# Optimization experiments

Hardware: AMD Instinct MI355X
Metric: run time of the kernel (lower is better)

## Reference

```python
import jax, jax.numpy as jnp
import numpy as np

D_MODEL = 512
EPS = 1e-5


def setup_inputs() -> dict:
    key = jax.random.key(0)
    k1, k2, k3 = jax.random.split(key, 3)
    B, N, D = 8, 2048, D_MODEL
    output = jax.random.normal(k1, (B, N, D), dtype=jnp.float32)
    # multiplicative 0/1 float mask over the [B, N, N] score matrix
    slf_attn_mask = jax.random.randint(k2, (B, N, N), 0, 2).astype(jnp.float32)
    # nn.Linear(d_model, d_model): weight [out, in], xavier-uniform; bias zeros-ish
    limit = float(np.sqrt(6.0 / (D + D)))
    W = jax.random.uniform(k3, (D, D), dtype=jnp.float32, minval=-limit, maxval=limit)
    b = jnp.zeros((D,), dtype=jnp.float32)
    return {"output": output, "slf_attn_mask": slf_attn_mask, "W": W, "b": b}


def reference(output, slf_attn_mask, W, b):
    temperature = jnp.asarray(D_MODEL, output.dtype) ** 0.5
    # scores: [B, N, N] = (q / temp) @ k^T, then multiplicative mask
    attn = jnp.einsum("bnd,bmd->bnm", output / temperature, output) * slf_attn_mask
    # F.normalize(p=2, dim=-1, eps=1e-5): x / max(||x||_2, eps)
    norm = jnp.sqrt(jnp.sum(attn * attn, axis=-1, keepdims=True))
    attn = attn / jnp.maximum(norm, EPS)
    # values: elu(Linear(output)), Linear uses W @ x + b with W [out, in]
    v = jax.nn.elu(jnp.einsum("bnd,ed->bne", output, W) + b)
    return jnp.einsum("bnm,bme->bne", attn, v)
```

## Files before the change

kernel.cpp:

```cpp
#include <hip/hip_runtime.h>
#include <hip/hip_bf16.h>

#define NSEQ 2048
#define DM 512
#define BATCH 8
#define GTOT (BATCH * NSEQ)
#define INV_T 0.044194173824159216f
#define EPSN 1e-5f

typedef __bf16 bf16_t;
typedef bf16_t bf16x8 __attribute__((ext_vector_type(8)));
typedef float f32x16 __attribute__((ext_vector_type(16)));
typedef unsigned short u16;
typedef unsigned int u32;
typedef unsigned char u8;
typedef unsigned long long u64;

__device__ __forceinline__ u16 f2bf(float f) {
    u32 u = __builtin_bit_cast(u32, f);
    u32 r = (u + 0x7FFFu + ((u >> 16) & 1u)) >> 16;
    return (u16)r;
}

__device__ __forceinline__ void async16(const u16* g, u16* l) {
    __builtin_amdgcn_global_load_lds(
        (const __attribute__((address_space(1))) u32*)g,
        (__attribute__((address_space(3))) u32*)l, 16, 0, 0);
}

__device__ __forceinline__ bf16x8 fragld64(const u16* t, int row, int kc) {
    return *(const bf16x8*)(t + row * 64 + ((kc ^ ((row >> 1) & 7)) << 3));
}

#define MFMA32(a, b, c) __builtin_amdgcn_mfma_f32_32x32x16_bf16(a, b, c, 0, 0, 0)
#define ROWOFF(reg, lh) (((reg) & 3) + 8 * ((reg) >> 2) + 4 * (lh))

#define STAGE64(Ag, ldA, Bg, ldB, k0)                                            \
    do {                                                                         \
        _Pragma("unroll") for (int j = 0; j < 4; ++j) {                          \
            const int cg = (lane & 7) ^ ((j * 4 + (lane >> 4)) & 7);             \
            const int dst = (wave * 4 + j) * 512 + lane * 8;                     \
            async16((Ag) + (long)(rS + j * 8) * (ldA) + (k0) + cg * 8, Ab + dst);\
            async16((Bg) + (long)(rS + j * 8) * (ldB) + (k0) + cg * 8, Bb + dst);\
        }                                                                        \
    } while (0)

__global__ __launch_bounds__(256) void k_convert(
    const float* __restrict__ X, const float* __restrict__ W,
    u16* __restrict__ Kbf, u16* __restrict__ Wbf, float* __restrict__ ssbuf) {
    const long NK = (long)GTOT * DM / 4;
    const long NW = (long)DM * DM / 4;
    const long NS = GTOT / 4;
    long i = (long)blockIdx.x * 256 + threadIdx.x;
    if (i < NK) {
        float4 f = ((const float4*)X)[i];
        ushort4 o;
        o.x = f2bf(f.x); o.y = f2bf(f.y); o.z = f2bf(f.z); o.w = f2bf(f.w);
        ((ushort4*)Kbf)[i] = o;
    } else if (i < NK + NW) {
        long j = i - NK;
        float4 f = ((const float4*)W)[j];
        ushort4 o;
        o.x = f2bf(f.x); o.y = f2bf(f.y); o.z = f2bf(f.z); o.w = f2bf(f.w);
        ((ushort4*)Wbf)[j] = o;
    } else if (i < NK + NW + NS) {
        ((float4*)ssbuf)[i - NK - NW] = (float4){0.f, 0.f, 0.f, 0.f};
    }
}

__global__ __launch_bounds__(256) void k_maskpack(
    const float* __restrict__ mask, u64* __restrict__ Mbits) {
    __shared__ u8 nib[256];
    const int tid = threadIdx.x;
    const long fbase = (long)blockIdx.x * 256 + tid;
    float4 f = ((const float4*)mask)[fbase];
    unsigned n = (f.x != 0.f ? 1u : 0u) | (f.y != 0.f ? 2u : 0u) |
                 (f.z != 0.f ? 4u : 0u) | (f.w != 0.f ? 8u : 0u);
    nib[tid] = (u8)n;
    __syncthreads();
    if (tid < 16) {
        u64 w = 0;
#pragma unroll
        for (int i = 0; i < 16; ++i) w |= (u64)nib[tid * 16 + i] << (i * 4);
        Mbits[(long)blockIdx.x * 16 + tid] = w;
    }
}

__global__ __launch_bounds__(256, 4) void k_sgemm(
    const u16* __restrict__ Kbf, const u32* __restrict__ Mw,
    u16* __restrict__ Sbuf, float* __restrict__ ssbuf) {
    __shared__ __attribute__((aligned(16))) u16 Ab[8192], Bb[8192];
    const int tid = threadIdx.x, wave = tid >> 6, lane = tid & 63;
    const int l31 = lane & 31, lh = lane >> 5;
    const int wy = wave >> 1, wx = wave & 1;
    const int b = blockIdx.z;
    const int M0 = blockIdx.y * 128, N0 = blockIdx.x * 128;
    const u16* Ag = Kbf + (long)(b * NSEQ + M0) * DM;
    const u16* Bg = Kbf + (long)(b * NSEQ + N0) * DM;
    const u32* Mb = Mw + (long)b * NSEQ * 64;

    const int rS = wave * 32 + (lane >> 3);

    f32x16 acc[2][2];
#pragma unroll
    for (int i = 0; i < 2; ++i)
#pragma unroll
        for (int j = 0; j < 2; ++j)
#pragma unroll
            for (int e = 0; e < 16; ++e) acc[i][j][e] = 0.f;

    for (int kt = 0; kt < 8; ++kt) {
        const int k0 = kt * 64;
        __syncthreads();
        STAGE64(Ag, DM, Bg, DM, k0);
        __syncthreads();
#pragma unroll
        for (int ks = 0; ks < 4; ++ks) {
            const int kc = ks * 2 + lh;
            bf16x8 a0 = fragld64(Ab, wy * 64 + l31, kc);
            bf16x8 a1 = fragld64(Ab, wy * 64 + 32 + l31, kc);
            bf16x8 b0 = fragld64(Bb, wx * 64 + l31, kc);
            bf16x8 b1 = fragld64(Bb, wx * 64 + 32 + l31, kc);
            acc[0][0] = MFMA32(a0, b0, acc[0][0]);
            acc[0][1] = MFMA32(a0, b1, acc[0][1]);
            acc[1][0] = MFMA32(a1, b0, acc[1][0]);
            acc[1][1] = MFMA32(a1, b1, acc[1][1]);
        }
    }
#pragma unroll
    for (int mi = 0; mi < 2; ++mi) {
#pragma unroll
        for (int reg = 0; reg < 16; ++reg) {
            int rl = M0 + wy * 64 + mi * 32 + ROWOFF(reg, lh);
            long rg = (long)b * NSEQ + rl;
            float v = 0.f;
#pragma unroll
            for (int ni = 0; ni < 2; ++ni) {
                int cg = N0 + wx * 64 + ni * 32 + l31;
                u32 w = Mb[(long)rl * 64 + (cg >> 5)];
                float s = ((w >> l31) & 1u) ? acc[mi][ni][reg] * INV_T : 0.f;
                v += s * s;
                Sbuf[rg * NSEQ + cg] = f2bf(s);
            }
            v += __shfl_xor(v, 1, 32);
            v += __shfl_xor(v, 2, 32);
            v += __shfl_xor(v, 4, 32);
            v += __shfl_xor(v, 8, 32);
            v += __shfl_xor(v, 16, 32);
            if (l31 == 0) atomicAdd(&ssbuf[rg], v);
        }
    }
}

__global__ __launch_bounds__(256, 4) void k_vgemm(
    const u16* __restrict__ Wbf, const u16* __restrict__ Kbf,
    const float* __restrict__ bias, u16* __restrict__ vT) {
    __shared__ __attribute__((aligned(16))) u16 Ab[8192], Bb[8192];
    const int tid = threadIdx.x, wave = tid >> 6, lane = tid & 63;
    const int l31 = lane & 31, lh = lane >> 5;
    const int wy = wave >> 1, wx = wave & 1;
    const int M0 = blockIdx.y * 128, N0 = blockIdx.x * 128;
    const u16* Ag = Wbf + (long)M0 * DM;
    const u16* Bg = Kbf + (long)N0 * DM;

    const int rS = wave * 32 + (lane >> 3);

    f32x16 acc[2][2];
#pragma unroll
    for (int i = 0; i < 2; ++i)
#pragma unroll
        for (int j = 0; j < 2; ++j)
#pragma unroll
            for (int e = 0; e < 16; ++e) acc[i][j][e] = 0.f;

    for (int kt = 0; kt < 8; ++kt) {
        const int k0 = kt * 64;
        __syncthreads();
        STAGE64(Ag, DM, Bg, DM, k0);
        __syncthreads();
#pragma unroll
        for (int ks = 0; ks < 4; ++ks) {
            const int kc = ks * 2 + lh;
            bf16x8 a0 = fragld64(Ab, wy * 64 + l31, kc);
            bf16x8 a1 = fragld64(Ab, wy * 64 + 32 + l31, kc);
            bf16x8 b0 = fragld64(Bb, wx * 64 + l31, kc);
            bf16x8 b1 = fragld64(Bb, wx * 64 + 32 + l31, kc);
            acc[0][0] = MFMA32(a0, b0, acc[0][0]);
            acc[0][1] = MFMA32(a0, b1, acc[0][1]);
            acc[1][0] = MFMA32(a1, b0, acc[1][0]);
            acc[1][1] = MFMA32(a1, b1, acc[1][1]);
        }
    }
#pragma unroll
    for (int mi = 0; mi < 2; ++mi) {
#pragma unroll
        for (int reg = 0; reg < 16; ++reg) {
            int e = M0 + wy * 64 + mi * 32 + ROWOFF(reg, lh);
            float bv = bias[e];
#pragma unroll
            for (int ni = 0; ni < 2; ++ni) {
                int g = N0 + wx * 64 + ni * 32 + l31;
                float x = acc[mi][ni][reg] + bv;
                float v = x > 0.f ? x : (__expf(x) - 1.f);
                vT[(long)e * GTOT + g] = f2bf(v);
            }
        }
    }
}

__global__ __launch_bounds__(256, 4) void k_pv(
    const u16* __restrict__ Sbuf, const u16* __restrict__ vT,
    const float* __restrict__ ssbuf, float* __restrict__ Out) {
    __shared__ __attribute__((aligned(16))) u16 Ab[8192], Bb[8192];
    __shared__ float sc[128];
    const int tid = threadIdx.x, wave = tid >> 6, lane = tid & 63;
    const int l31 = lane & 31, lh = lane >> 5;
    const int wy = wave >> 1, wx = wave & 1;
    const int b = blockIdx.z;
    const int M0 = blockIdx.y * 128, N0 = blockIdx.x * 128;
    const u16* Ag = Sbuf + (long)(b * NSEQ + M0) * NSEQ;
    const u16* Bg = vT + (long)N0 * GTOT + b * NSEQ;

    if (tid < 128) {
        float v = ssbuf[b * NSEQ + M0 + tid];
        sc[tid] = 1.f / fmaxf(sqrtf(v), EPSN);
    }

    const int rS = wave * 32 + (lane >> 3);

    f32x16 acc[2][2];
#pragma unroll
    for (int i = 0; i < 2; ++i)
#pragma unroll
        for (int j = 0; j < 2; ++j)
#pragma unroll
            for (int e = 0; e < 16; ++e) acc[i][j][e] = 0.f;

    for (int kt = 0; kt < 32; ++kt) {
        const int k0 = kt * 64;
        __syncthreads();
        STAGE64(Ag, NSEQ, Bg, GTOT, k0);
        __syncthreads();
#pragma unroll
        for (int ks = 0; ks < 4; ++ks) {
            const int kc = ks * 2 + lh;
            bf16x8 a0 = fragld64(Ab, wy * 64 + l31, kc);
            bf16x8 a1 = fragld64(Ab, wy * 64 + 32 + l31, kc);
            bf16x8 b0 = fragld64(Bb, wx * 64 + l31, kc);
            bf16x8 b1 = fragld64(Bb, wx * 64 + 32 + l31, kc);
            acc[0][0] = MFMA32(a0, b0, acc[0][0]);
            acc[0][1] = MFMA32(a0, b1, acc[0][1]);
            acc[1][0] = MFMA32(a1, b0, acc[1][0]);
            acc[1][1] = MFMA32(a1, b1, acc[1][1]);
        }
    }
#pragma unroll
    for (int mi = 0; mi < 2; ++mi) {
#pragma unroll
        for (int reg = 0; reg < 16; ++reg) {
            int rl = wy * 64 + mi * 32 + ROWOFF(reg, lh);
            float s = sc[rl];
            float* op = Out + ((long)b * NSEQ + M0 + rl) * DM;
#pragma unroll
            for (int ni = 0; ni < 2; ++ni) {
                int d = N0 + wx * 64 + ni * 32 + l31;
                op[d] = acc[mi][ni][reg] * s;
            }
        }
    }
}

extern "C" void kernel_launch(void* const* d_in, const int* in_sizes, int n_in,
                              void* d_out, int out_size, void* d_ws, size_t ws_size,
                              hipStream_t stream) {
    const float* X = (const float*)d_in[0];
    const float* mask = (const float*)d_in[1];
    const float* W = (const float*)d_in[2];
    const float* bias = (const float*)d_in[3];
    float* out = (float*)d_out;

    char* ws = (char*)d_ws;
    u16* Kbf = (u16*)ws;
    u16* Wbf = (u16*)(ws + 16777216);
    u16* vT = (u16*)(ws + 17301504);
    u16* Sbuf = (u16*)(ws + 34078720);
    float* ssbuf = (float*)(ws + 101187584);
    u64* Mbits = (u64*)(ws + 101253120);

    k_convert<<<8464, 256, 0, stream>>>(X, W, Kbf, Wbf, ssbuf);
    k_maskpack<<<32768, 256, 0, stream>>>(mask, Mbits);
    k_vgemm<<<dim3(128, 4), 256, 0, stream>>>(Wbf, Kbf, bias, vT);
    k_sgemm<<<dim3(16, 16, 8), 256, 0, stream>>>(Kbf, (const u32*)Mbits, Sbuf, ssbuf);
    k_pv<<<dim3(4, 16, 8), 256, 0, stream>>>(Sbuf, vT, ssbuf, out);
}
```

Baseline: 347.8 us.

## Fuse score GEMM, masking, row-norm and PV GEMM into one kernel

Replaces the separate score GEMM and PV GEMM kernels with a single fused kernel where each block holds 64 query rows in LDS, computes masked scores for 256-key chunks, stages them as bf16 in LDS, and immediately multiplies by V. Row sums of squares are accumulated in registers and reduced across waves at the end, removing the global score buffer round-trip and the atomics. The trade-off is a grid of only 256 large blocks with K and V fragments loaded directly from global memory without double buffering, which may expose latency.

Measured after the change: 396.1 us. 1.14x slower.

```diff
diff --git a/kernel.cpp b/kernel.cpp
--- a/kernel.cpp
+++ b/kernel.cpp
@@ -47,10 +47,9 @@
 
 __global__ __launch_bounds__(256) void k_convert(
     const float* __restrict__ X, const float* __restrict__ W,
-    u16* __restrict__ Kbf, u16* __restrict__ Wbf, float* __restrict__ ssbuf) {
+    u16* __restrict__ Kbf, u16* __restrict__ Wbf) {
     const long NK = (long)GTOT * DM / 4;
     const long NW = (long)DM * DM / 4;
-    const long NS = GTOT / 4;
     long i = (long)blockIdx.x * 256 + threadIdx.x;
     if (i < NK) {
         float4 f = ((const float4*)X)[i];
@@ -63,8 +62,6 @@
         ushort4 o;
         o.x = f2bf(f.x); o.y = f2bf(f.y); o.z = f2bf(f.z); o.w = f2bf(f.w);
         ((ushort4*)Wbf)[j] = o;
-    } else if (i < NK + NW + NS) {
-        ((float4*)ssbuf)[i - NK - NW] = (float4){0.f, 0.f, 0.f, 0.f};
     }
 }
 
@@ -86,18 +83,16 @@
     }
 }
 
-__global__ __launch_bounds__(256, 4) void k_sgemm(
-    const u16* __restrict__ Kbf, const u32* __restrict__ Mw,
-    u16* __restrict__ Sbuf, float* __restrict__ ssbuf) {
+__global__ __launch_bounds__(256, 4) void k_vgemm(
+    const u16* __restrict__ Wbf, const u16* __restrict__ Kbf,
+    const float* __restrict__ bias, u16* __restrict__ vT) {
     __shared__ __attribute__((aligned(16))) u16 Ab[8192], Bb[8192];
     const int tid = threadIdx.x, wave = tid >> 6, lane = tid & 63;
     const int l31 = lane & 31, lh = lane >> 5;
     const int wy = wave >> 1, wx = wave & 1;
-    const int b = blockIdx.z;
     const int M0 = blockIdx.y * 128, N0 = blockIdx.x * 128;
-    const u16* Ag = Kbf + (long)(b * NSEQ + M0) * DM;
-    const u16* Bg = Kbf + (long)(b * NSEQ + N0) * DM;
-    const u32* Mb = Mw + (long)b * NSEQ * 64;
+    const u16* Ag = Wbf + (long)M0 * DM;
+    const u16* Bg = Kbf + (long)N0 * DM;
 
     const int rS = wave * 32 + (lane >> 3);
 
@@ -131,70 +126,6 @@
     for (int mi = 0; mi < 2; ++mi) {
 #pragma unroll
         for (int reg = 0; reg < 16; ++reg) {
-            int rl = M0 + wy * 64 + mi * 32 + ROWOFF(reg, lh);
-            long rg = (long)b * NSEQ + rl;
-            float v = 0.f;
-#pragma unroll
-            for (int ni = 0; ni < 2; ++ni) {
-                int cg = N0 + wx * 64 + ni * 32 + l31;
-                u32 w = Mb[(long)rl * 64 + (cg >> 5)];
-                float s = ((w >> l31) & 1u) ? acc[mi][ni][reg] * INV_T : 0.f;
-                v += s * s;
-                Sbuf[rg * NSEQ + cg] = f2bf(s);
-            }
-            v += __shfl_xor(v, 1, 32);
-            v += __shfl_xor(v, 2, 32);
-            v += __shfl_xor(v, 4, 32);
-            v += __shfl_xor(v, 8, 32);
-            v += __shfl_xor(v, 16, 32);
-            if (l31 == 0) atomicAdd(&ssbuf[rg], v);
-        }
-    }
-}
-
-__global__ __launch_bounds__(256, 4) void k_vgemm(
-    const u16* __restrict__ Wbf, const u16* __restrict__ Kbf,
-    const float* __restrict__ bias, u16* __restrict__ vT) {
-    __shared__ __attribute__((aligned(16))) u16 Ab[8192], Bb[8192];
-    const int tid = threadIdx.x, wave = tid >> 6, lane = tid & 63;
-    const int l31 = lane & 31, lh = lane >> 5;
-    const int wy = wave >> 1, wx = wave & 1;
-    const int M0 = blockIdx.y * 128, N0 = blockIdx.x * 128;
-    const u16* Ag = Wbf + (long)M0 * DM;
-    const u16* Bg = Kbf + (long)N0 * DM;
-
-    const int rS = wave * 32 + (lane >> 3);
-
-    f32x16 acc[2][2];
-#pragma unroll
-    for (int i = 0; i < 2; ++i)
-#pragma unroll
-        for (int j = 0; j < 2; ++j)
-#pragma unroll
-            for (int e = 0; e < 16; ++e) acc[i][j][e] = 0.f;
-
-    for (int kt = 0; kt < 8; ++kt) {
-        const int k0 = kt * 64;
-        __syncthreads();
-        STAGE64(Ag, DM, Bg, DM, k0);
-        __syncthreads();
-#pragma unroll
-        for (int ks = 0; ks < 4; ++ks) {
-            const int kc = ks * 2 + lh;
-            bf16x8 a0 = fragld64(Ab, wy * 64 + l31, kc);
-            bf16x8 a1 = fragld64(Ab, wy * 64 + 32 + l31, kc);
-            bf16x8 b0 = fragld64(Bb, wx * 64 + l31, kc);
-            bf16x8 b1 = fragld64(Bb, wx * 64 + 32 + l31, kc);
-            acc[0][0] = MFMA32(a0, b0, acc[0][0]);
-            acc[0][1] = MFMA32(a0, b1, acc[0][1]);
-            acc[1][0] = MFMA32(a1, b0, acc[1][0]);
-            acc[1][1] = MFMA32(a1, b1, acc[1][1]);
-        }
-    }
-#pragma unroll
-    for (int mi = 0; mi < 2; ++mi) {
-#pragma unroll
-        for (int reg = 0; reg < 16; ++reg) {
             int e = M0 + wy * 64 + mi * 32 + ROWOFF(reg, lh);
             float bv = bias[e];
 #pragma unroll
@@ -208,64 +139,132 @@
     }
 }
 
-__global__ __launch_bounds__(256, 4) void k_pv(
-    const u16* __restrict__ Sbuf, const u16* __restrict__ vT,
-    const float* __restrict__ ssbuf, float* __restrict__ Out) {
-    __shared__ __attribute__((aligned(16))) u16 Ab[8192], Bb[8192];
-    __shared__ float sc[128];
-    const int tid = threadIdx.x, wave = tid >> 6, lane = tid & 63;
-    const int l31 = lane & 31, lh = lane >> 5;
-    const int wy = wave >> 1, wx = wave & 1;
-    const int b = blockIdx.z;
-    const int M0 = blockIdx.y * 128, N0 = blockIdx.x * 128;
-    const u16* Ag = Sbuf + (long)(b * NSEQ + M0) * NSEQ;
-    const u16* Bg = vT + (long)N0 * GTOT + b * NSEQ;
-
-    if (tid < 128) {
-        float v = ssbuf[b * NSEQ + M0 + tid];
-        sc[tid] = 1.f / fmaxf(sqrtf(v), EPSN);
-    }
-
-    const int rS = wave * 32 + (lane >> 3);
-
-    f32x16 acc[2][2];
+__global__ __launch_bounds__(512, 2) void k_fused(
+    const u16* __restrict__ Kbf, const u16* __restrict__ vT,
+    const u32* __restrict__ Mw, float* __restrict__ Out) {
+    __shared__ __attribute__((aligned(16))) u16 Qb[64 * 512];
+    __shared__ __attribute__((aligned(16))) u16 Sb[64 * 256];
+    __shared__ float ssred[8][64];
+    __shared__ float ssinv[64];
+
+    const int tid = threadIdx.x;
+    const int w = tid >> 6, lane = tid & 63, l31 = lane & 31, lh = lane >> 5;
+    const int b = blockIdx.x & 7, q = blockIdx.x >> 3;
+    const int M0 = q * 64;
+    const long rowbase = (long)b * NSEQ + M0;
+
+    {
+        const u16* src = Kbf + rowbase * DM;
+#pragma unroll
+        for (int it = 0; it < 8; ++it) {
+            int idx = it * 512 + tid;
+            int row = idx >> 6, cd = idx & 63;
+            int cg = cd ^ (row & 31);
+            async16(src + (long)row * DM + cg * 8, Qb + idx * 8);
+        }
+    }
+
+    f32x16 oc[2][2];
 #pragma unroll
     for (int i = 0; i < 2; ++i)
 #pragma unroll
         for (int j = 0; j < 2; ++j)
 #pragma unroll
-            for (int e = 0; e < 16; ++e) acc[i][j][e] = 0.f;
-
-    for (int kt = 0; kt < 32; ++kt) {
-        const int k0 = kt * 64;
-        __syncthreads();
-        STAGE64(Ag, NSEQ, Bg, GTOT, k0);
-        __syncthreads();
-#pragma unroll
-        for (int ks = 0; ks < 4; ++ks) {
-            const int kc = ks * 2 + lh;
-            bf16x8 a0 = fragld64(Ab, wy * 64 + l31, kc);
-            bf16x8 a1 = fragld64(Ab, wy * 64 + 32 + l31, kc);
-            bf16x8 b0 = fragld64(Bb, wx * 64 + l31, kc);
-            bf16x8 b1 = fragld64(Bb, wx * 64 + 32 + l31, kc);
-            acc[0][0] = MFMA32(a0, b0, acc[0][0]);
-            acc[0][1] = MFMA32(a0, b1, acc[0][1]);
-            acc[1][0] = MFMA32(a1, b0, acc[1][0]);
-            acc[1][1] = MFMA32(a1, b1, acc[1][1]);
-        }
-    }
-#pragma unroll
-    for (int mi = 0; mi < 2; ++mi) {
+            for (int e = 0; e < 16; ++e) oc[i][j][e] = 0.f;
+
+    float ss[32];
+#pragma unroll
+    for (int i = 0; i < 32; ++i) ss[i] = 0.f;
+
+    const u16* kp = Kbf + ((long)b * NSEQ + 32 * w + l31) * DM + lh * 8;
+    const u16* vp0 = vT + (long)(64 * w + l31) * GTOT + (long)b * NSEQ + lh * 8;
+    const u16* vp1 = vp0 + (long)32 * GTOT;
+    const u32* Mb = Mw + rowbase * 64;
+
+    __syncthreads();
+
+#pragma unroll 1
+    for (int t = 0; t < 8; ++t) {
+        const int kv0 = t * 256;
+        f32x16 p0, p1;
+#pragma unroll
+        for (int e = 0; e < 16; ++e) { p0[e] = 0.f; p1[e] = 0.f; }
+        const u16* kpt = kp + (long)kv0 * DM;
+#pragma unroll
+        for (int ks = 0; ks < 32; ++ks) {
+            bf16x8 bk = *(const bf16x8*)(kpt + ks * 16);
+            const int sl = ((2 * ks + lh) ^ l31) << 3;
+            bf16x8 a0 = *(const bf16x8*)(Qb + l31 * DM + sl);
+            bf16x8 a1 = *(const bf16x8*)(Qb + (32 + l31) * DM + sl);
+            p0 = MFMA32(a0, bk, p0);
+            p1 = MFMA32(a1, bk, p1);
+        }
+        __syncthreads();
+        const int col = 32 * w + l31;
+        const u32* mb = Mb + t * 8 + w;
+#pragma unroll
+        for (int sr = 0; sr < 2; ++sr) {
+#pragma unroll
+            for (int reg = 0; reg < 16; ++reg) {
+                const int row = 32 * sr + ROWOFF(reg, lh);
+                u32 mwd = mb[row * 64];
+                float s = ((mwd >> l31) & 1u) ? (sr ? p1[reg] : p0[reg]) * INV_T : 0.f;
+                ss[sr * 16 + reg] += s * s;
+                int cw = (col >> 3) ^ (row & 31);
+                Sb[row * 256 + cw * 8 + (col & 7)] = f2bf(s);
+            }
+        }
+        __syncthreads();
+#pragma unroll
+        for (int ks = 0; ks < 16; ++ks) {
+            const int sl = ((2 * ks + lh) ^ l31) << 3;
+            bf16x8 a0 = *(const bf16x8*)(Sb + l31 * 256 + sl);
+            bf16x8 a1 = *(const bf16x8*)(Sb + (32 + l31) * 256 + sl);
+            bf16x8 v0 = *(const bf16x8*)(vp0 + kv0 + ks * 16);
+            bf16x8 v1 = *(const bf16x8*)(vp1 + kv0 + ks * 16);
+            oc[0][0] = MFMA32(a0, v0, oc[0][0]);
+            oc[0][1] = MFMA32(a0, v1, oc[0][1]);
+            oc[1][0] = MFMA32(a1, v0, oc[1][0]);
+            oc[1][1] = MFMA32(a1, v1, oc[1][1]);
+        }
+    }
+
+#pragma unroll
+    for (int i = 0; i < 32; ++i) {
+        float v = ss[i];
+        v += __shfl_xor(v, 1, 32);
+        v += __shfl_xor(v, 2, 32);
+        v += __shfl_xor(v, 4, 32);
+        v += __shfl_xor(v, 8, 32);
+        v += __shfl_xor(v, 16, 32);
+        ss[i] = v;
+    }
+    if (l31 == 0) {
+#pragma unroll
+        for (int sr = 0; sr < 2; ++sr)
+#pragma unroll
+            for (int reg = 0; reg < 16; ++reg)
+                ssred[w][32 * sr + ROWOFF(reg, lh)] = ss[sr * 16 + reg];
+    }
+    __syncthreads();
+    if (tid < 64) {
+        float v = 0.f;
+#pragma unroll
+        for (int j = 0; j < 8; ++j) v += ssred[j][tid];
+        ssinv[tid] = 1.f / fmaxf(sqrtf(v), EPSN);
+    }
+    __syncthreads();
+
+    float* ob = Out + rowbase * DM;
+#pragma unroll
+    for (int ms = 0; ms < 2; ++ms) {
 #pragma unroll
         for (int reg = 0; reg < 16; ++reg) {
-            int rl = wy * 64 + mi * 32 + ROWOFF(reg, lh);
-            float s = sc[rl];
-            float* op = Out + ((long)b * NSEQ + M0 + rl) * DM;
-#pragma unroll
-            for (int ni = 0; ni < 2; ++ni) {
-                int d = N0 + wx * 64 + ni * 32 + l31;
-                op[d] = acc[mi][ni][reg] * s;
-            }
+            const int row = 32 * ms + ROWOFF(reg, lh);
+            const float scl = ssinv[row];
+            float* op = ob + (long)row * DM + 64 * w + l31;
+            __builtin_nontemporal_store(oc[ms][0][reg] * scl, op);
+            __builtin_nontemporal_store(oc[ms][1][reg] * scl, op + 32);
         }
     }
 }
@@ -283,13 +282,10 @@
     u16* Kbf = (u16*)ws;
     u16* Wbf = (u16*)(ws + 16777216);
     u16* vT = (u16*)(ws + 17301504);
-    u16* Sbuf = (u16*)(ws + 34078720);
-    float* ssbuf = (float*)(ws + 101187584);
     u64* Mbits = (u64*)(ws + 101253120);
 
-    k_convert<<<8464, 256, 0, stream>>>(X, W, Kbf, Wbf, ssbuf);
+    k_convert<<<8448, 256, 0, stream>>>(X, W, Kbf, Wbf);
     k_maskpack<<<32768, 256, 0, stream>>>(mask, Mbits);
     k_vgemm<<<dim3(128, 4), 256, 0, stream>>>(Wbf, Kbf, bias, vT);
-    k_sgemm<<<dim3(16, 16, 8), 256, 0, stream>>>(Kbf, (const u32*)Mbits, Sbuf, ssbuf);
-    k_pv<<<dim3(4, 16, 8), 256, 0, stream>>>(Sbuf, vT, ssbuf, out);
-}
+    k_fused<<<256, 512, 0, stream>>>(Kbf, vT, (const u32*)Mbits, out);
+}
```

## Double-buffer S-GEMM with 256x256 tiles, 8 waves, and split async staging

Applied to the files above, without the earlier changes.

Reworks the score GEMM kernel to use 256x256 output tiles with 512 threads (8 waves, each computing 128x64) and double-buffered LDS, 128 KB in total. The next K-slice's A and B loads are issued around the MFMA phases and gated with explicit vmcnt waits and raw barriers, so global loads overlap compute and the per-iteration double syncthreads goes away. It also raises MFMA wave priority, uses a 1D grid with batch in the low bits, and writes scores with nontemporal stores. The large LDS footprint and register use limit occupancy, and the hand-placed waits depend on exact counts of outstanding loads.

Result: slower. 391.2 us (+12.5%).

```diff
diff --git a/kernel.cpp b/kernel.cpp
--- a/kernel.cpp
+++ b/kernel.cpp
@@ -35,6 +35,9 @@
 #define MFMA32(a, b, c) __builtin_amdgcn_mfma_f32_32x32x16_bf16(a, b, c, 0, 0, 0)
 #define ROWOFF(reg, lh) (((reg) & 3) + 8 * ((reg) >> 2) + 4 * (lh))
 
+#define BAR() asm volatile("s_barrier" ::: "memory")
+#define VMCNT(n) asm volatile("s_waitcnt vmcnt(" #n ")" ::: "memory")
+
 #define STAGE64(Ag, ldA, Bg, ldB, k0)                                            \
     do {                                                                         \
         _Pragma("unroll") for (int j = 0; j < 4; ++j) {                          \
@@ -42,6 +45,38 @@
             const int dst = (wave * 4 + j) * 512 + lane * 8;                     \
             async16((Ag) + (long)(rS + j * 8) * (ldA) + (k0) + cg * 8, Ab + dst);\
             async16((Bg) + (long)(rS + j * 8) * (ldB) + (k0) + cg * 8, Bb + dst);\
+        }                                                                        \
+    } while (0)
+
+#define STG(g, ld, k0, dst)                                                      \
+    do {                                                                         \
+        _Pragma("unroll") for (int j = 0; j < 4; ++j) {                          \
+            const int cg = (lane & 7) ^ ((j * 4 + (lane >> 4)) & 7);             \
+            async16((g) + (long)(rS + j * 8) * (ld) + (k0) + cg * 8,             \
+                    (dst) + (wave * 4 + j) * 512 + lane * 8);                    \
+        }                                                                        \
+    } while (0)
+
+#define QPHASE(Ac, Bc, ks0)                                                      \
+    do {                                                                         \
+        _Pragma("unroll") for (int ks = (ks0); ks < (ks0) + 2; ++ks) {           \
+            const int kc = ks * 2 + lh;                                          \
+            bf16x8 b0 = fragld64((Bc), wx * 64 + l31, kc);                       \
+            bf16x8 b1 = fragld64((Bc), wx * 64 + 32 + l31, kc);                  \
+            bf16x8 a0 = fragld64((Ac), wy * 128 + l31, kc);                      \
+            bf16x8 a1 = fragld64((Ac), wy * 128 + 32 + l31, kc);                 \
+            bf16x8 a2 = fragld64((Ac), wy * 128 + 64 + l31, kc);                 \
+            bf16x8 a3 = fragld64((Ac), wy * 128 + 96 + l31, kc);                 \
+            __builtin_amdgcn_s_setprio(1);                                       \
+            acc[0][0] = MFMA32(a0, b0, acc[0][0]);                               \
+            acc[0][1] = MFMA32(a0, b1, acc[0][1]);                               \
+            acc[1][0] = MFMA32(a1, b0, acc[1][0]);                               \
+            acc[1][1] = MFMA32(a1, b1, acc[1][1]);                               \
+            acc[2][0] = MFMA32(a2, b0, acc[2][0]);                               \
+            acc[2][1] = MFMA32(a2, b1, acc[2][1]);                               \
+            acc[3][0] = MFMA32(a3, b0, acc[3][0]);                               \
+            acc[3][1] = MFMA32(a3, b1, acc[3][1]);                               \
+            __builtin_amdgcn_s_setprio(0);                                       \
         }                                                                        \
     } while (0)
 
@@ -86,61 +121,72 @@
     }
 }
 
-__global__ __launch_bounds__(256, 4) void k_sgemm(
+__global__ __launch_bounds__(512, 2) void k_sgemm(
     const u16* __restrict__ Kbf, const u32* __restrict__ Mw,
     u16* __restrict__ Sbuf, float* __restrict__ ssbuf) {
-    __shared__ __attribute__((aligned(16))) u16 Ab[8192], Bb[8192];
+    __shared__ __attribute__((aligned(16))) u16 Sm[65536];
+    u16* A0 = Sm;
+    u16* B0 = Sm + 16384;
+    u16* A1 = Sm + 32768;
+    u16* B1 = Sm + 49152;
+
     const int tid = threadIdx.x, wave = tid >> 6, lane = tid & 63;
     const int l31 = lane & 31, lh = lane >> 5;
-    const int wy = wave >> 1, wx = wave & 1;
-    const int b = blockIdx.z;
-    const int M0 = blockIdx.y * 128, N0 = blockIdx.x * 128;
+    const int wy = wave >> 2, wx = wave & 3;
+    const int bid = blockIdx.x;
+    const int b = bid & 7;
+    const int ty = (bid >> 3) & 7, tx = bid >> 6;
+    const int M0 = ty * 256, N0 = tx * 256;
     const u16* Ag = Kbf + (long)(b * NSEQ + M0) * DM;
     const u16* Bg = Kbf + (long)(b * NSEQ + N0) * DM;
     const u32* Mb = Mw + (long)b * NSEQ * 64;
 
     const int rS = wave * 32 + (lane >> 3);
 
-    f32x16 acc[2][2];
-#pragma unroll
-    for (int i = 0; i < 2; ++i)
+    f32x16 acc[4][2];
+#pragma unroll
+    for (int i = 0; i < 4; ++i)
 #pragma unroll
         for (int j = 0; j < 2; ++j)
 #pragma unroll
             for (int e = 0; e < 16; ++e) acc[i][j][e] = 0.f;
 
-    for (int kt = 0; kt < 8; ++kt) {
-        const int k0 = kt * 64;
-        __syncthreads();
-        STAGE64(Ag, DM, Bg, DM, k0);
-        __syncthreads();
-#pragma unroll
-        for (int ks = 0; ks < 4; ++ks) {
-            const int kc = ks * 2 + lh;
-            bf16x8 a0 = fragld64(Ab, wy * 64 + l31, kc);
-            bf16x8 a1 = fragld64(Ab, wy * 64 + 32 + l31, kc);
-            bf16x8 b0 = fragld64(Bb, wx * 64 + l31, kc);
-            bf16x8 b1 = fragld64(Bb, wx * 64 + 32 + l31, kc);
-            acc[0][0] = MFMA32(a0, b0, acc[0][0]);
-            acc[0][1] = MFMA32(a0, b1, acc[0][1]);
-            acc[1][0] = MFMA32(a1, b0, acc[1][0]);
-            acc[1][1] = MFMA32(a1, b1, acc[1][1]);
-        }
-    }
-#pragma unroll
-    for (int mi = 0; mi < 2; ++mi) {
+    STG(Ag, DM, 0, A0);
+    STG(Bg, DM, 0, B0);
+
+#pragma unroll
+    for (int t = 0; t < 8; ++t) {
+        u16* Ac = (t & 1) ? A1 : A0;
+        u16* Bc = (t & 1) ? B1 : B0;
+        u16* An = (t & 1) ? A0 : A1;
+        u16* Bn = (t & 1) ? B0 : B1;
+        if (t < 7) {
+            STG(Ag, DM, (t + 1) * 64, An);
+            VMCNT(4);
+        } else {
+            VMCNT(0);
+        }
+        BAR();
+        QPHASE(Ac, Bc, 0);
+        if (t < 7) STG(Bg, DM, (t + 1) * 64, Bn);
+        QPHASE(Ac, Bc, 2);
+        BAR();
+    }
+
+#pragma unroll
+    for (int rt = 0; rt < 4; ++rt) {
 #pragma unroll
         for (int reg = 0; reg < 16; ++reg) {
-            int rl = M0 + wy * 64 + mi * 32 + ROWOFF(reg, lh);
+            int rl = M0 + wy * 128 + rt * 32 + ROWOFF(reg, lh);
             long rg = (long)b * NSEQ + rl;
             float v = 0.f;
 #pragma unroll
-            for (int ni = 0; ni < 2; ++ni) {
-                int cg = N0 + wx * 64 + ni * 32 + l31;
+            for (int ct = 0; ct < 2; ++ct) {
+                int cg = N0 + wx * 64 + ct * 32 + l31;
                 u32 w = Mb[(long)rl * 64 + (cg >> 5)];
-                float s = ((w >> l31) & 1u) ? acc[mi][ni][reg] * INV_T : 0.f;
+                float s = ((w >> l31) & 1u) ? acc[rt][ct][reg] * INV_T : 0.f;
                 v += s * s;
-                Sbuf[rg * NSEQ + cg] = f2bf(s);
+                __builtin_nontemporal_store(f2bf(s), &Sbuf[rg * NSEQ + cg]);
             }
             v += __shfl_xor(v, 1, 32);
             v += __shfl_xor(v, 2, 32);
@@ -290,6 +336,6 @@
     k_convert<<<8464, 256, 0, stream>>>(X, W, Kbf, Wbf, ssbuf);
     k_maskpack<<<32768, 256, 0, stream>>>(mask, Mbits);
     k_vgemm<<<dim3(128, 4), 256, 0, stream>>>(Wbf, Kbf, bias, vT);
-    k_sgemm<<<dim3(16, 16, 8), 256, 0, stream>>>(Kbf, (const u32*)Mbits, Sbuf, ssbuf);
+    k_sgemm<<<512, 512, 0, stream>>>(Kbf, (const u32*)Mbits, Sbuf, ssbuf);
     k_pv<<<dim3(4, 16, 8), 256, 0, stream>>>(Sbuf, vT, ssbuf, out);
 }
```

## Fuse mask read into score GEMM epilogue and remap block order for batch interleave

Applied to the files above, without the earlier changes.

Removes the separate mask bit-packing kernel: the score GEMM epilogue now multiplies by the float mask read directly from global memory. This saves one kernel launch and the extra pass over the 128 MB mask, at the cost of reading the full fp32 mask in the GEMM epilogue, which could become bandwidth-bound there. Both GEMMs also switch to a 1D grid with the batch index in the low bits, so consecutive blocks are spread across batches. The aim is better L2/XCD locality and scheduling of the tiles.

New measurement: 333.6 us. 4.1% less time.

```diff
diff --git a/kernel.cpp b/kernel.cpp
--- a/kernel.cpp
+++ b/kernel.cpp
@@ -13,7 +13,6 @@
 typedef float f32x16 __attribute__((ext_vector_type(16)));
 typedef unsigned short u16;
 typedef unsigned int u32;
-typedef unsigned char u8;
 typedef unsigned long long u64;
 
 __device__ __forceinline__ u16 f2bf(float f) {
@@ -68,36 +67,19 @@
     }
 }
 
-__global__ __launch_bounds__(256) void k_maskpack(
-    const float* __restrict__ mask, u64* __restrict__ Mbits) {
-    __shared__ u8 nib[256];
-    const int tid = threadIdx.x;
-    const long fbase = (long)blockIdx.x * 256 + tid;
-    float4 f = ((const float4*)mask)[fbase];
-    unsigned n = (f.x != 0.f ? 1u : 0u) | (f.y != 0.f ? 2u : 0u) |
-                 (f.z != 0.f ? 4u : 0u) | (f.w != 0.f ? 8u : 0u);
-    nib[tid] = (u8)n;
-    __syncthreads();
-    if (tid < 16) {
-        u64 w = 0;
-#pragma unroll
-        for (int i = 0; i < 16; ++i) w |= (u64)nib[tid * 16 + i] << (i * 4);
-        Mbits[(long)blockIdx.x * 16 + tid] = w;
-    }
-}
-
 __global__ __launch_bounds__(256, 4) void k_sgemm(
-    const u16* __restrict__ Kbf, const u32* __restrict__ Mw,
+    const u16* __restrict__ Kbf, const float* __restrict__ mask,
     u16* __restrict__ Sbuf, float* __restrict__ ssbuf) {
     __shared__ __attribute__((aligned(16))) u16 Ab[8192], Bb[8192];
     const int tid = threadIdx.x, wave = tid >> 6, lane = tid & 63;
     const int l31 = lane & 31, lh = lane >> 5;
     const int wy = wave >> 1, wx = wave & 1;
-    const int b = blockIdx.z;
-    const int M0 = blockIdx.y * 128, N0 = blockIdx.x * 128;
+    const int bid = blockIdx.x;
+    const int b = bid & 7;
+    const int ty = (bid >> 3) & 15, tx = bid >> 7;
+    const int M0 = ty * 128, N0 = tx * 128;
     const u16* Ag = Kbf + (long)(b * NSEQ + M0) * DM;
     const u16* Bg = Kbf + (long)(b * NSEQ + N0) * DM;
-    const u32* Mb = Mw + (long)b * NSEQ * 64;
 
     const int rS = wave * 32 + (lane >> 3);
 
@@ -133,12 +115,12 @@
         for (int reg = 0; reg < 16; ++reg) {
             int rl = M0 + wy * 64 + mi * 32 + ROWOFF(reg, lh);
             long rg = (long)b * NSEQ + rl;
+            const float* mrow = mask + rg * NSEQ;
             float v = 0.f;
 #pragma unroll
             for (int ni = 0; ni < 2; ++ni) {
                 int cg = N0 + wx * 64 + ni * 32 + l31;
-                u32 w = Mb[(long)rl * 64 + (cg >> 5)];
-                float s = ((w >> l31) & 1u) ? acc[mi][ni][reg] * INV_T : 0.f;
+                float s = acc[mi][ni][reg] * INV_T * mrow[cg];
                 v += s * s;
                 Sbuf[rg * NSEQ + cg] = f2bf(s);
             }
@@ -216,8 +198,11 @@
     const int tid = threadIdx.x, wave = tid >> 6, lane = tid & 63;
     const int l31 = lane & 31, lh = lane >> 5;
     const int wy = wave >> 1, wx = wave & 1;
-    const int b = blockIdx.z;
-    const int M0 = blockIdx.y * 128, N0 = blockIdx.x * 128;
+    const int bid = blockIdx.x;
+    const int b = bid & 7;
+    const int r = bid >> 3;
+    const int tx = r & 3, ty = r >> 2;
+    const int M0 = ty * 128, N0 = tx * 128;
     const u16* Ag = Sbuf + (long)(b * NSEQ + M0) * NSEQ;
     const u16* Bg = vT + (long)N0 * GTOT + b * NSEQ;
 
@@ -285,11 +270,9 @@
     u16* vT = (u16*)(ws + 17301504);
     u16* Sbuf = (u16*)(ws + 34078720);
     float* ssbuf = (float*)(ws + 101187584);
-    u64* Mbits = (u64*)(ws + 101253120);
 
     k_convert<<<8464, 256, 0, stream>>>(X, W, Kbf, Wbf, ssbuf);
-    k_maskpack<<<32768, 256, 0, stream>>>(mask, Mbits);
     k_vgemm<<<dim3(128, 4), 256, 0, stream>>>(Wbf, Kbf, bias, vT);
-    k_sgemm<<<dim3(16, 16, 8), 256, 0, stream>>>(Kbf, (const u32*)Mbits, Sbuf, ssbuf);
-    k_pv<<<dim3(4, 16, 8), 256, 0, stream>>>(Sbuf, vT, ssbuf, out);
-}
+    k_sgemm<<<2048, 256, 0, stream>>>(Kbf, mask, Sbuf, ssbuf);
+    k_pv<<<512, 256, 0, stream>>>(Sbuf, vT, ssbuf, out);
+}
```
